# Optimization experiments

Measured on AMD Instinct MI355X. Metric: run time of the kernel, lower is better.

Reference implementation:

```python
import jax, jax.numpy as jnp
import numpy as np

# Model dims (Mamba-130M style)
BATCH, SEQ = 2, 1024
D_MODEL = 768
D_INNER = 1536          # 2 * d_model
DT_RANK = 48            # ceil(d_model / 16)
N_STATE = 16
D_CONV = 4
N_LAYER = 2
VOCAB = 50304           # 50257 padded to multiple of 64


def rms_norm(x, eps=1e-6):
    return x * jax.lax.rsqrt(jnp.mean(x * x, axis=-1, keepdims=True) + eps)


def setup_inputs():
    key = jax.random.key(0)
    ks = jax.random.split(key, 10)
    s = 3 ** 0.5 * D_MODEL ** -0.5
    si = 3 ** 0.5 * D_INNER ** -0.5
    # dt_proj bias init (inverse-softplus of dt in [1e-3, 1e-1]) as in init_weights
    u = jax.random.uniform(ks[6], (N_LAYER, D_INNER))
    dt = jnp.exp(u * (np.log(0.1) - np.log(0.001)) + np.log(0.001))
    dt = jnp.clip(dt, 1e-4)
    dt_proj_b = dt + jnp.log(-jnp.expm1(-dt))
    A_log = jnp.tile(jnp.log(jnp.arange(1, N_STATE + 1, dtype=jnp.float32)), (N_LAYER, D_INNER, 1))
    return {
        "tokens": jax.random.randint(ks[0], (BATCH, SEQ), 0, VOCAB),
        "wte": jax.random.normal(ks[1], (VOCAB, D_MODEL), dtype=jnp.float32) * 0.02,
        "in_proj_w": jax.random.uniform(ks[2], (N_LAYER, 2 * D_INNER, D_MODEL), minval=-s, maxval=s),
        "conv_w": jax.random.normal(ks[3], (N_LAYER, D_INNER, 1, D_CONV)) * 0.2,
        "conv_b": jnp.zeros((N_LAYER, D_INNER)),
        "x_proj_w": jax.random.uniform(ks[4], (N_LAYER, DT_RANK + 2 * N_STATE, D_INNER), minval=-si, maxval=si),
        "dt_proj_w": jax.random.uniform(ks[5], (N_LAYER, D_INNER, DT_RANK), minval=-DT_RANK ** -0.5, maxval=DT_RANK ** -0.5),
        "dt_proj_b": dt_proj_b,
        "out_proj_w": jax.random.normal(ks[7], (N_LAYER, D_MODEL, D_INNER)) * si * 0.1,
        "A_log": A_log,
        "D": jnp.ones((N_LAYER, D_INNER)),
        "lm_head_w": jax.random.normal(ks[8], (VOCAB, D_MODEL)) * 0.001,
    }


def _scan_combine(e1, e2):
    a1, b1 = e1
    a2, b2 = e2
    return (a1 * a2, a2 * b1 + b2)


def selective_scan(x, dt, A, Bs, Cs, Dp):
    # x, dt: (B,L,Di); A: (Di,N); Bs, Cs: (B,L,N); Dp: (Di,)
    dA = jnp.exp(dt[..., None] * A)                       # (B,L,Di,N)
    dBx = dt[..., None] * Bs[:, :, None, :] * x[..., None]  # (B,L,Di,N)
    _, h = jax.lax.associative_scan(_scan_combine, (dA, dBx), axis=1)
    y = jnp.einsum('bldn,bln->bld', h, Cs)
    return y + Dp * x


def _mixer(h, in_w, cw, cb, xp_w, dtp_w, dtp_b, out_w, A_log, Dp):
    xz = h @ in_w.T                                      # (B,L,2*Di)
    x, z = jnp.split(xz, 2, axis=-1)
    xc = jnp.transpose(x, (0, 2, 1))                     # (B,Di,L)
    xc = jax.lax.conv_general_dilated(
        xc, cw, window_strides=(1,), padding=[(D_CONV - 1, 0)],
        feature_group_count=D_INNER,
        dimension_numbers=('NCH', 'OIH', 'NCH')) + cb[None, :, None]
    x = jax.nn.silu(jnp.transpose(xc, (0, 2, 1)))        # (B,L,Di)
    x_dbl = x @ xp_w.T                                   # (B,L,dt_rank+2N)
    dt, Bs, Cs = jnp.split(x_dbl, [DT_RANK, DT_RANK + N_STATE], axis=-1)
    dt = jax.nn.softplus(dt @ dtp_w.T + dtp_b)
    A = -jnp.exp(A_log)
    y = selective_scan(x, dt, A, Bs, Cs, Dp)
    return (y * jax.nn.silu(z)) @ out_w.T


def reference(tokens, wte, in_proj_w, conv_w, conv_b, x_proj_w, dt_proj_w,
              dt_proj_b, out_proj_w, A_log, D, lm_head_w):
    x = wte[tokens]                                      # (B,L,D)
    for i in range(in_proj_w.shape[0]):
        x = x + _mixer(rms_norm(x), in_proj_w[i], conv_w[i], conv_b[i],
                       x_proj_w[i], dt_proj_w[i], dt_proj_b[i],
                       out_proj_w[i], A_log[i], D[i])
    x = rms_norm(x)
    return x @ lm_head_w.T                               # (B,L,VOCAB)
```

## Files before the change

### kernel.cpp

```cpp
#include <hip/hip_runtime.h>
#include <hip/hip_bf16.h>

#define BATCH 2
#define SEQ 1024
#define DMODEL 768
#define DINNER 1536
#define DTRANK 48
#define NSTATE 16
#define NLAYER 2
#define VOCAB 50304
#define NTOK (BATCH * SEQ)

typedef __attribute__((ext_vector_type(8))) short short8;
typedef __attribute__((ext_vector_type(4))) float f32x4;

__device__ __forceinline__ unsigned short f2bf(float f) {
    union { float f; unsigned u; } v; v.f = f;
    unsigned r = v.u + 0x7fffu + ((v.u >> 16) & 1u);
    return (unsigned short)(r >> 16);
}

__global__ __launch_bounds__(256) void cvt_bf16_kernel(const float* __restrict__ in,
                                                       unsigned short* __restrict__ out,
                                                       int n8) {
    int i = blockIdx.x * 256 + threadIdx.x;
    if (i >= n8) return;
    const float4* p = (const float4*)in + 2 * (size_t)i;
    float4 a = p[0], b = p[1];
    union { unsigned short us[8]; uint4 v; } o;
    o.us[0] = f2bf(a.x); o.us[1] = f2bf(a.y); o.us[2] = f2bf(a.z); o.us[3] = f2bf(a.w);
    o.us[4] = f2bf(b.x); o.us[5] = f2bf(b.y); o.us[6] = f2bf(b.z); o.us[7] = f2bf(b.w);
    ((uint4*)out)[i] = o.v;
}

template <int EPI>
__global__ __launch_bounds__(256) void gemm_bf16(const unsigned short* __restrict__ A, int lda,
                                                 const unsigned short* __restrict__ B, int ldb,
                                                 float* __restrict__ C, int ldc,
                                                 int K) {
    __shared__ unsigned short As[128 * 32];
    __shared__ unsigned short Bs[128 * 32];
    const int tid = threadIdx.x;
    const int lane = tid & 63;
    const int wave = tid >> 6;
    const int m0 = blockIdx.y * 128;
    const int n0 = blockIdx.x * 128;
    const int wr = (wave >> 1) * 64;
    const int wc = (wave & 1) * 64;

    f32x4 acc[4][4] = {};

    for (int k0 = 0; k0 < K; k0 += 32) {
        __syncthreads();
        #pragma unroll
        for (int j = 0; j < 2; ++j) {
            int c = j * 256 + tid;
            int row = c >> 2;
            int kc = (c & 3) * 8;
            __builtin_amdgcn_global_load_lds(
                (const __attribute__((address_space(1))) unsigned int*)(A + (size_t)(m0 + row) * lda + k0 + kc),
                (__attribute__((address_space(3))) unsigned int*)(As + c * 8), 16, 0, 0);
            __builtin_amdgcn_global_load_lds(
                (const __attribute__((address_space(1))) unsigned int*)(B + (size_t)(n0 + row) * ldb + k0 + kc),
                (__attribute__((address_space(3))) unsigned int*)(Bs + c * 8), 16, 0, 0);
        }
        __syncthreads();

        short8 a[4], b[4];
        #pragma unroll
        for (int i = 0; i < 4; ++i)
            a[i] = *(const short8*)(As + (wr + i * 16 + (lane & 15)) * 32 + (lane >> 4) * 8);
        #pragma unroll
        for (int i = 0; i < 4; ++i)
            b[i] = *(const short8*)(Bs + (wc + i * 16 + (lane & 15)) * 32 + (lane >> 4) * 8);
        #pragma unroll
        for (int i = 0; i < 4; ++i)
            #pragma unroll
            for (int j = 0; j < 4; ++j)
                acc[i][j] = __builtin_amdgcn_mfma_f32_16x16x32_bf16(a[i], b[j], acc[i][j], 0, 0, 0);
    }

    const int row_base = m0 + wr + (lane >> 4) * 4;
    const int col_base = n0 + wc + (lane & 15);
    #pragma unroll
    for (int i = 0; i < 4; ++i)
        #pragma unroll
        for (int j = 0; j < 4; ++j)
            #pragma unroll
            for (int q = 0; q < 4; ++q) {
                size_t idx = (size_t)(row_base + i * 16 + q) * ldc + col_base + j * 16;
                if (EPI == 0) C[idx] = acc[i][j][q];
                else          C[idx] += acc[i][j][q];
            }
}

__global__ __launch_bounds__(256) void embed_kernel(const int* __restrict__ tokens,
                                                    const float* __restrict__ wte,
                                                    float* __restrict__ x) {
    int gid = blockIdx.x * 256 + threadIdx.x;
    int t = gid / (DMODEL / 4);
    int c = gid % (DMODEL / 4);
    if (t >= NTOK) return;
    int tok = tokens[t];
    ((float4*)x)[t * (DMODEL / 4) + c] = ((const float4*)wte)[(size_t)tok * (DMODEL / 4) + c];
}

__global__ __launch_bounds__(256) void rmsnorm_kernel(const float* __restrict__ in,
                                                      float* __restrict__ out) {
    int row = blockIdx.x;
    int tid = threadIdx.x;
    const float* r = in + row * DMODEL;
    float v0 = r[tid], v1 = r[tid + 256], v2 = r[tid + 512];
    float s = v0 * v0 + v1 * v1 + v2 * v2;
    #pragma unroll
    for (int off = 32; off > 0; off >>= 1) s += __shfl_down(s, off);
    __shared__ float red[4];
    int wid = tid >> 6, lane = tid & 63;
    if (lane == 0) red[wid] = s;
    __syncthreads();
    if (tid == 0) {
        float tot = red[0] + red[1] + red[2] + red[3];
        red[0] = 1.0f / sqrtf(tot / (float)DMODEL + 1e-6f);
    }
    __syncthreads();
    float sc = red[0];
    float* o = out + row * DMODEL;
    o[tid] = v0 * sc; o[tid + 256] = v1 * sc; o[tid + 512] = v2 * sc;
}

template <int EPI>
__global__ __launch_bounds__(256) void gemm_tn(const float* __restrict__ A, int lda,
                                               const float* __restrict__ B, int ldb,
                                               float* __restrict__ C, int ldc,
                                               int M, int N, int K,
                                               const float* __restrict__ bias) {
    __shared__ float As[16][68];
    __shared__ float Bs[16][68];
    const int tid = threadIdx.x;
    const int m0 = blockIdx.y * 64;
    const int n0 = blockIdx.x * 64;
    const int lr = tid >> 2;
    const int lq = (tid & 3) * 4;
    const int tm = (tid & 15) * 4;
    const int tn = (tid >> 4) * 4;
    float acc[4][4] = {};

    for (int k0 = 0; k0 < K; k0 += 16) {
        float4 av = *(const float4*)(A + (m0 + lr) * lda + k0 + lq);
        float4 bv = make_float4(0.f, 0.f, 0.f, 0.f);
        if (n0 + lr < N) bv = *(const float4*)(B + (n0 + lr) * ldb + k0 + lq);
        __syncthreads();
        As[lq + 0][lr] = av.x; As[lq + 1][lr] = av.y; As[lq + 2][lr] = av.z; As[lq + 3][lr] = av.w;
        Bs[lq + 0][lr] = bv.x; Bs[lq + 1][lr] = bv.y; Bs[lq + 2][lr] = bv.z; Bs[lq + 3][lr] = bv.w;
        __syncthreads();
        #pragma unroll
        for (int kk = 0; kk < 16; ++kk) {
            float4 a = *(const float4*)&As[kk][tm];
            float4 b = *(const float4*)&Bs[kk][tn];
            const float* ap = (const float*)&a;
            const float* bp = (const float*)&b;
            #pragma unroll
            for (int i = 0; i < 4; ++i)
                #pragma unroll
                for (int j = 0; j < 4; ++j)
                    acc[i][j] = fmaf(ap[i], bp[j], acc[i][j]);
        }
    }

    #pragma unroll
    for (int i = 0; i < 4; ++i) {
        int m = m0 + tm + i;
        #pragma unroll
        for (int j = 0; j < 4; ++j) {
            int n = n0 + tn + j;
            if (n >= N) continue;
            float v = acc[i][j];
            if (EPI == 0) {
                C[m * ldc + n] = v;
            } else {
                v += bias[n];
                C[m * ldc + n] = (v > 20.f) ? v : log1pf(expf(v));
            }
        }
    }
}

__global__ __launch_bounds__(256) void conv_silu_kernel(const float* __restrict__ xz,
                                                        const float* __restrict__ cw,
                                                        const float* __restrict__ cb,
                                                        float* __restrict__ xs) {
    int gid = blockIdx.x * 256 + threadIdx.x;
    int d = gid % DINNER;
    int t = gid / DINNER;
    if (t >= NTOK) return;
    int l = t & (SEQ - 1);
    int tb = t - l;
    float4 w = ((const float4*)cw)[d];
    const float* wp = (const float*)&w;
    float acc = cb[d];
    #pragma unroll
    for (int k = 0; k < 4; ++k) {
        int lk = l - 3 + k;
        float v = (lk >= 0) ? xz[(tb + lk) * (2 * DINNER) + d] : 0.f;
        acc = fmaf(wp[k], v, acc);
    }
    xs[t * DINNER + d] = acc / (1.f + expf(-acc));
}

__global__ __launch_bounds__(256) void transpose2_kernel(const float* __restrict__ dtb,
                                                         const float* __restrict__ xs,
                                                         float* __restrict__ dt_t,
                                                         float* __restrict__ xs_t) {
    __shared__ float t0[32][33];
    __shared__ float t1[32][33];
    const int tid = threadIdx.x;
    const int tx = tid & 31, ty = tid >> 5;
    const int tbase = blockIdx.x * 32;
    const int dbase = blockIdx.y * 32;
    #pragma unroll
    for (int i = 0; i < 4; ++i) {
        int t = tbase + ty + i * 8;
        t0[ty + i * 8][tx] = dtb[(size_t)t * DINNER + dbase + tx];
        t1[ty + i * 8][tx] = xs[(size_t)t * DINNER + dbase + tx];
    }
    __syncthreads();
    const int b = tbase >> 10;
    const int l0 = tbase & (SEQ - 1);
    #pragma unroll
    for (int i = 0; i < 4; ++i) {
        int d = dbase + ty + i * 8;
        size_t o = (size_t)(b * DINNER + d) * SEQ + l0 + tx;
        dt_t[o] = t0[tx][ty + i * 8];
        xs_t[o] = t1[tx][ty + i * 8];
    }
}

__global__ __launch_bounds__(256) void scan2_kernel(const float* __restrict__ dt_t,
                                                    const float* __restrict__ x_t,
                                                    const float* __restrict__ xdbl,
                                                    const float* __restrict__ A_log,
                                                    const float* __restrict__ Dp,
                                                    float* __restrict__ y_t) {
    const int bd = blockIdx.x;
    const int d = bd % DINNER;
    const int b = bd / DINNER;
    const int tid = threadIdx.x;
    const int c = tid >> 4;
    const int n = tid & 15;

    const float* dtp = dt_t + (size_t)bd * SEQ + c * 64;
    const float* xp  = x_t  + (size_t)bd * SEQ + c * 64;
    const float* xd  = xdbl + (size_t)(b * SEQ + c * 64) * 80;
    const float A = -expf(A_log[d * NSTATE + n]);

    float a = 1.f, h = 0.f;
    #pragma unroll 4
    for (int q = 0; q < 16; ++q) {
        float4 dq = ((const float4*)dtp)[q];
        float4 xq = ((const float4*)xp)[q];
        const float* dv = (const float*)&dq;
        const float* xv = (const float*)&xq;
        #pragma unroll
        for (int j = 0; j < 4; ++j) {
            int l = q * 4 + j;
            float Bv = xd[l * 80 + DTRANK + n];
            float dA = expf(dv[j] * A);
            a *= dA;
            h = fmaf(h, dA, dv[j] * Bv * xv[j]);
        }
    }

    __shared__ float sa[16][16];
    __shared__ float sb[16][16];
    sa[c][n] = a; sb[c][n] = h;
    __syncthreads();
    if (tid < 16) {
        float hrun = 0.f;
        #pragma unroll
        for (int cc = 0; cc < 16; ++cc) {
            float av = sa[cc][tid];
            float bv = sb[cc][tid];
            sa[cc][tid] = hrun;
            hrun = fmaf(av, hrun, bv);
        }
    }
    __syncthreads();

    float hh = sa[c][n];
    const float Dv = Dp[d];
    float* yo = y_t + (size_t)bd * SEQ + c * 64;
    #pragma unroll 4
    for (int q = 0; q < 16; ++q) {
        float4 dq = ((const float4*)dtp)[q];
        float4 xq = ((const float4*)xp)[q];
        const float* dv = (const float*)&dq;
        const float* xv = (const float*)&xq;
        #pragma unroll
        for (int j = 0; j < 4; ++j) {
            int l = q * 4 + j;
            float Bv = xd[l * 80 + DTRANK + n];
            float Cv = xd[l * 80 + DTRANK + NSTATE + n];
            float dA = expf(dv[j] * A);
            hh = fmaf(hh, dA, dv[j] * Bv * xv[j]);
            float p = hh * Cv;
            p += __shfl_xor(p, 1, 16);
            p += __shfl_xor(p, 2, 16);
            p += __shfl_xor(p, 4, 16);
            p += __shfl_xor(p, 8, 16);
            if (n == 0) yo[l] = fmaf(Dv, xv[j], p);
        }
    }
}

__global__ __launch_bounds__(256) void gate_tr_kernel(const float* __restrict__ y_t,
                                                      const float* __restrict__ xz,
                                                      unsigned short* __restrict__ g) {
    __shared__ float ty_[32][33];
    const int tid = threadIdx.x;
    const int tx = tid & 31, ty = tid >> 5;
    const int tbase = blockIdx.x * 32;
    const int dbase = blockIdx.y * 32;
    const int b = tbase >> 10;
    const int l0 = tbase & (SEQ - 1);
    #pragma unroll
    for (int i = 0; i < 4; ++i) {
        int d = dbase + ty + i * 8;
        ty_[ty + i * 8][tx] = y_t[(size_t)(b * DINNER + d) * SEQ + l0 + tx];
    }
    __syncthreads();
    #pragma unroll
    for (int i = 0; i < 4; ++i) {
        int t = tbase + ty + i * 8;
        int d = dbase + tx;
        float z = xz[(size_t)t * (2 * DINNER) + DINNER + d];
        float yv = ty_[tx][ty + i * 8];
        float gv = yv * z / (1.f + expf(-z));
        g[(size_t)t * DINNER + d] = f2bf(gv);
    }
}

extern "C" void kernel_launch(void* const* d_in, const int* in_sizes, int n_in,
                              void* d_out, int out_size, void* d_ws, size_t ws_size,
                              hipStream_t stream) {
    const int*   tokens     = (const int*)d_in[0];
    const float* wte        = (const float*)d_in[1];
    const float* in_proj_w  = (const float*)d_in[2];
    const float* conv_w     = (const float*)d_in[3];
    const float* conv_b     = (const float*)d_in[4];
    const float* x_proj_w   = (const float*)d_in[5];
    const float* dt_proj_w  = (const float*)d_in[6];
    const float* dt_proj_b  = (const float*)d_in[7];
    const float* out_proj_w = (const float*)d_in[8];
    const float* A_log      = (const float*)d_in[9];
    const float* Dparam     = (const float*)d_in[10];
    const float* lm_head_w  = (const float*)d_in[11];
    float* out = (float*)d_out;

    float* ws   = (float*)d_ws;
    float* x    = ws;
    float* xn   = x    + NTOK * DMODEL;
    float* xz   = xn   + NTOK * DMODEL;
    float* xs   = xz   + NTOK * 2 * DINNER;
    float* xdbl = xs   + NTOK * DINNER;
    float* dtb  = xdbl + NTOK * 80;
    float* dt_t = dtb  + NTOK * DINNER;
    float* xs_t = dt_t + NTOK * DINNER;
    float* y_t  = xs_t + NTOK * DINNER;
    unsigned short* xnb   = (unsigned short*)(y_t + NTOK * DINNER);
    unsigned short* gb    = xnb   + NTOK * DMODEL;
    unsigned short* inwb  = gb    + NTOK * DINNER;
    unsigned short* outwb = inwb  + 2 * 2 * DINNER * DMODEL;
    unsigned short* lmwb  = outwb + 2 * DMODEL * DINNER;

    {
        int n8 = 2 * 2 * DINNER * DMODEL / 8;
        cvt_bf16_kernel<<<(n8 + 255) / 256, 256, 0, stream>>>(in_proj_w, inwb, n8);
        n8 = 2 * DMODEL * DINNER / 8;
        cvt_bf16_kernel<<<(n8 + 255) / 256, 256, 0, stream>>>(out_proj_w, outwb, n8);
        n8 = VOCAB * DMODEL / 8;
        cvt_bf16_kernel<<<(n8 + 255) / 256, 256, 0, stream>>>(lm_head_w, lmwb, n8);
    }

    embed_kernel<<<NTOK * (DMODEL / 4) / 256, 256, 0, stream>>>(tokens, wte, x);

    for (int i = 0; i < NLAYER; ++i) {
        const unsigned short* inw = inwb + (size_t)i * 2 * DINNER * DMODEL;
        const float* cw   = conv_w     + (size_t)i * DINNER * 4;
        const float* cb   = conv_b     + (size_t)i * DINNER;
        const float* xpw  = x_proj_w   + (size_t)i * (DTRANK + 2 * NSTATE) * DINNER;
        const float* dtpw = dt_proj_w  + (size_t)i * DINNER * DTRANK;
        const float* dtpb = dt_proj_b  + (size_t)i * DINNER;
        const unsigned short* outw = outwb + (size_t)i * DMODEL * DINNER;
        const float* alog = A_log      + (size_t)i * DINNER * NSTATE;
        const float* dpar = Dparam     + (size_t)i * DINNER;

        rmsnorm_kernel<<<NTOK, 256, 0, stream>>>(x, xn);
        cvt_bf16_kernel<<<NTOK * DMODEL / 8 / 256, 256, 0, stream>>>(xn, xnb, NTOK * DMODEL / 8);
        gemm_bf16<0><<<dim3(2 * DINNER / 128, NTOK / 128), 256, 0, stream>>>(
            xnb, DMODEL, inw, DMODEL, xz, 2 * DINNER, DMODEL);
        conv_silu_kernel<<<NTOK * DINNER / 256, 256, 0, stream>>>(xz, cw, cb, xs);
        gemm_tn<0><<<dim3(2, NTOK / 64), 256, 0, stream>>>(
            xs, DINNER, xpw, DINNER, xdbl, 80, NTOK, 80, DINNER, nullptr);
        gemm_tn<1><<<dim3(DINNER / 64, NTOK / 64), 256, 0, stream>>>(
            xdbl, 80, dtpw, DTRANK, dtb, DINNER, NTOK, DINNER, DTRANK, dtpb);
        transpose2_kernel<<<dim3(NTOK / 32, DINNER / 32), 256, 0, stream>>>(dtb, xs, dt_t, xs_t);
        scan2_kernel<<<BATCH * DINNER, 256, 0, stream>>>(dt_t, xs_t, xdbl, alog, dpar, y_t);
        gate_tr_kernel<<<dim3(NTOK / 32, DINNER / 32), 256, 0, stream>>>(y_t, xz, gb);
        gemm_bf16<2><<<dim3(DMODEL / 128, NTOK / 128), 256, 0, stream>>>(
            gb, DINNER, outw, DINNER, x, DMODEL, DINNER);
    }

    rmsnorm_kernel<<<NTOK, 256, 0, stream>>>(x, xn);
    cvt_bf16_kernel<<<NTOK * DMODEL / 8 / 256, 256, 0, stream>>>(xn, xnb, NTOK * DMODEL / 8);
    gemm_bf16<0><<<dim3(VOCAB / 128, NTOK / 128), 256, 0, stream>>>(
        xnb, DMODEL, lmwb, DMODEL, out, VOCAB, DMODEL);
}
```

Before: 1.402 ms.

## Fuse RMSNorm with bf16 cast and remap GEMM tiles across XCDs

RMSNorm now writes bf16 directly, which removes the separate fp32 normalized buffer and the conversion kernel before each bf16 GEMM. The bf16 GEMM switches to a 1D grid with an XCD-aware workgroup remap. Consecutive tiles that share the same B column block (M-fastest ordering) are placed on the same XCD to improve L2 reuse, mainly for the large LM-head GEMM. Loop variables are renamed to avoid shadowing the new q variable.

```diff
diff --git a/kernel.cpp b/kernel.cpp
--- a/kernel.cpp
+++ b/kernel.cpp
@@ -37,14 +37,20 @@
 __global__ __launch_bounds__(256) void gemm_bf16(const unsigned short* __restrict__ A, int lda,
                                                  const unsigned short* __restrict__ B, int ldb,
                                                  float* __restrict__ C, int ldc,
-                                                 int K) {
+                                                 int K, int mtiles) {
+    const int nwg = gridDim.x;
+    const int bid = blockIdx.x;
+    const int q = nwg >> 3, r = nwg & 7;
+    const int xcd = bid & 7, loc = bid >> 3;
+    const int wgid = (xcd < r ? xcd * (q + 1) : r * (q + 1) + (xcd - r) * q) + loc;
+    const int m0 = (wgid % mtiles) * 128;
+    const int n0 = (wgid / mtiles) * 128;
+
     __shared__ unsigned short As[128 * 32];
     __shared__ unsigned short Bs[128 * 32];
     const int tid = threadIdx.x;
     const int lane = tid & 63;
     const int wave = tid >> 6;
-    const int m0 = blockIdx.y * 128;
-    const int n0 = blockIdx.x * 128;
     const int wr = (wave >> 1) * 64;
     const int wc = (wave & 1) * 64;
 
@@ -87,10 +93,10 @@
         #pragma unroll
         for (int j = 0; j < 4; ++j)
             #pragma unroll
-            for (int q = 0; q < 4; ++q) {
-                size_t idx = (size_t)(row_base + i * 16 + q) * ldc + col_base + j * 16;
-                if (EPI == 0) C[idx] = acc[i][j][q];
-                else          C[idx] += acc[i][j][q];
+            for (int q2 = 0; q2 < 4; ++q2) {
+                size_t idx = (size_t)(row_base + i * 16 + q2) * ldc + col_base + j * 16;
+                if (EPI == 0) C[idx] = acc[i][j][q2];
+                else          C[idx] += acc[i][j][q2];
             }
 }
 
@@ -105,8 +111,8 @@
     ((float4*)x)[t * (DMODEL / 4) + c] = ((const float4*)wte)[(size_t)tok * (DMODEL / 4) + c];
 }
 
-__global__ __launch_bounds__(256) void rmsnorm_kernel(const float* __restrict__ in,
-                                                      float* __restrict__ out) {
+__global__ __launch_bounds__(256) void rmsnorm_bf16_kernel(const float* __restrict__ in,
+                                                           unsigned short* __restrict__ out) {
     int row = blockIdx.x;
     int tid = threadIdx.x;
     const float* r = in + row * DMODEL;
@@ -124,8 +130,8 @@
     }
     __syncthreads();
     float sc = red[0];
-    float* o = out + row * DMODEL;
-    o[tid] = v0 * sc; o[tid + 256] = v1 * sc; o[tid + 512] = v2 * sc;
+    unsigned short* o = out + row * DMODEL;
+    o[tid] = f2bf(v0 * sc); o[tid + 256] = f2bf(v1 * sc); o[tid + 512] = f2bf(v2 * sc);
 }
 
 template <int EPI>
@@ -255,14 +261,14 @@
 
     float a = 1.f, h = 0.f;
     #pragma unroll 4
-    for (int q = 0; q < 16; ++q) {
-        float4 dq = ((const float4*)dtp)[q];
-        float4 xq = ((const float4*)xp)[q];
+    for (int qq = 0; qq < 16; ++qq) {
+        float4 dq = ((const float4*)dtp)[qq];
+        float4 xq = ((const float4*)xp)[qq];
         const float* dv = (const float*)&dq;
         const float* xv = (const float*)&xq;
         #pragma unroll
         for (int j = 0; j < 4; ++j) {
-            int l = q * 4 + j;
+            int l = qq * 4 + j;
             float Bv = xd[l * 80 + DTRANK + n];
             float dA = expf(dv[j] * A);
             a *= dA;
@@ -290,14 +296,14 @@
     const float Dv = Dp[d];
     float* yo = y_t + (size_t)bd * SEQ + c * 64;
     #pragma unroll 4
-    for (int q = 0; q < 16; ++q) {
-        float4 dq = ((const float4*)dtp)[q];
-        float4 xq = ((const float4*)xp)[q];
+    for (int qq = 0; qq < 16; ++qq) {
+        float4 dq = ((const float4*)dtp)[qq];
+        float4 xq = ((const float4*)xp)[qq];
         const float* dv = (const float*)&dq;
         const float* xv = (const float*)&xq;
         #pragma unroll
         for (int j = 0; j < 4; ++j) {
-            int l = q * 4 + j;
+            int l = qq * 4 + j;
             float Bv = xd[l * 80 + DTRANK + n];
             float Cv = xd[l * 80 + DTRANK + NSTATE + n];
             float dA = expf(dv[j] * A);
@@ -358,8 +364,7 @@
 
     float* ws   = (float*)d_ws;
     float* x    = ws;
-    float* xn   = x    + NTOK * DMODEL;
-    float* xz   = xn   + NTOK * DMODEL;
+    float* xz   = x    + NTOK * DMODEL;
     float* xs   = xz   + NTOK * 2 * DINNER;
     float* xdbl = xs   + NTOK * DINNER;
     float* dtb  = xdbl + NTOK * 80;
@@ -394,10 +399,9 @@
         const float* alog = A_log      + (size_t)i * DINNER * NSTATE;
         const float* dpar = Dparam     + (size_t)i * DINNER;
 
-        rmsnorm_kernel<<<NTOK, 256, 0, stream>>>(x, xn);
-        cvt_bf16_kernel<<<NTOK * DMODEL / 8 / 256, 256, 0, stream>>>(xn, xnb, NTOK * DMODEL / 8);
-        gemm_bf16<0><<<dim3(2 * DINNER / 128, NTOK / 128), 256, 0, stream>>>(
-            xnb, DMODEL, inw, DMODEL, xz, 2 * DINNER, DMODEL);
+        rmsnorm_bf16_kernel<<<NTOK, 256, 0, stream>>>(x, xnb);
+        gemm_bf16<0><<<(NTOK / 128) * (2 * DINNER / 128), 256, 0, stream>>>(
+            xnb, DMODEL, inw, DMODEL, xz, 2 * DINNER, DMODEL, NTOK / 128);
         conv_silu_kernel<<<NTOK * DINNER / 256, 256, 0, stream>>>(xz, cw, cb, xs);
         gemm_tn<0><<<dim3(2, NTOK / 64), 256, 0, stream>>>(
             xs, DINNER, xpw, DINNER, xdbl, 80, NTOK, 80, DINNER, nullptr);
@@ -406,12 +410,11 @@
         transpose2_kernel<<<dim3(NTOK / 32, DINNER / 32), 256, 0, stream>>>(dtb, xs, dt_t, xs_t);
         scan2_kernel<<<BATCH * DINNER, 256, 0, stream>>>(dt_t, xs_t, xdbl, alog, dpar, y_t);
         gate_tr_kernel<<<dim3(NTOK / 32, DINNER / 32), 256, 0, stream>>>(y_t, xz, gb);
-        gemm_bf16<2><<<dim3(DMODEL / 128, NTOK / 128), 256, 0, stream>>>(
-            gb, DINNER, outw, DINNER, x, DMODEL, DINNER);
-    }
-
-    rmsnorm_kernel<<<NTOK, 256, 0, stream>>>(x, xn);
-    cvt_bf16_kernel<<<NTOK * DMODEL / 8 / 256, 256, 0, stream>>>(xn, xnb, NTOK * DMODEL / 8);
-    gemm_bf16<0><<<dim3(VOCAB / 128, NTOK / 128), 256, 0, stream>>>(
-        xnb, DMODEL, lmwb, DMODEL, out, VOCAB, DMODEL);
-}
+        gemm_bf16<2><<<(NTOK / 128) * (DMODEL / 128), 256, 0, stream>>>(
+            gb, DINNER, outw, DINNER, x, DMODEL, DINNER, NTOK / 128);
+    }
+
+    rmsnorm_bf16_kernel<<<NTOK, 256, 0, stream>>>(x, xnb);
+    gemm_bf16<0><<<(NTOK / 128) * (VOCAB / 128), 256, 0, stream>>>(
+        xnb, DMODEL, lmwb, DMODEL, out, VOCAB, DMODEL, NTOK / 128);
+}
```

Result: no change. 1.379 ms (-1.7%).
